# Performance work log

Measured on AMD Instinct MI355X. Metric: run time of the kernel, lower is better.

Reference implementation:

```python
import jax, jax.numpy as jnp
import numpy as np

N_HEADS = 8
N_LAYERS = 2
LN_EPS = 1e-5


def _mha(x, Win, bin_, Wout, bout):
    # torch nn.MultiheadAttention, eval mode (dropout off). x: [b, s, d]
    b, s, d = x.shape
    dh = d // N_HEADS
    qkv = x @ Win.T + bin_                      # [b, s, 3d]
    q, k, v = jnp.split(qkv, 3, axis=-1)
    q = q.reshape(b, s, N_HEADS, dh)
    k = k.reshape(b, s, N_HEADS, dh)
    v = v.reshape(b, s, N_HEADS, dh)
    scores = jnp.einsum('bqhd,bkhd->bhqk', q, k) / jnp.sqrt(jnp.asarray(dh, x.dtype))
    attn = jax.nn.softmax(scores, axis=-1)
    o = jnp.einsum('bhqk,bkhd->bqhd', attn, v).reshape(b, s, d)
    return o @ Wout.T + bout


def _layer_norm(x, g, b):
    mu = jnp.mean(x, axis=-1, keepdims=True)
    var = jnp.mean(jnp.square(x - mu), axis=-1, keepdims=True)
    return (x - mu) * jax.lax.rsqrt(var + LN_EPS) * g + b


def _vertex_conv(feat, inc, prev, Win, bin_, Wout, bout, Wproj, ln_g, ln_b, alpha):
    # feat: [b,m,d], inc: [b,m,e]
    attn = _mha(feat, Win, bin_, Wout, bout)              # [b,m,d]
    scores = jnp.einsum('bme,bmd->bed', inc, attn)        # incidence aggregation
    w = jax.nn.softmax(scores, axis=1)                    # softmax over edges
    # fused form of einsum('bme,bmd->bmed') then einsum('bmed,bed->bed')
    edge = scores * w                                     # [b,e,d]
    edge = edge @ Wproj.T                                 # no-bias projection
    edge = _layer_norm(edge, ln_g, ln_b)
    if prev is not None:
        edge = alpha * prev + (1.0 - alpha) * edge
        edge = edge + prev
    return edge


def _edge_conv(inc, edge_feat, prev, Win, bin_, Wout, bout, Wproj, ln_g, ln_b, alpha):
    # inc: [b,m,e], edge_feat: [b,e,d]
    _ = _mha(edge_feat, Win, bin_, Wout, bout)            # attn computed, output unused downstream
    wef = jnp.einsum('bed,bme->bmd', edge_feat, inc)      # edge->node aggregation
    node = wef @ Wproj.T
    node = _layer_norm(node, ln_g, ln_b)
    if prev is not None:
        node = alpha * prev + (1.0 - alpha) * node
        node = node + prev
    return node


def setup_inputs() -> dict:
    key = jax.random.key(0)
    ks = jax.random.split(key, 8)
    b, m, e, d = 8, 1024, 1536, 256
    s = 0.02
    return {
        'features': jax.random.normal(ks[0], (b, m, d), jnp.float32),
        'inc_mat': (jax.random.uniform(ks[1], (b, m, e), jnp.float32) < 0.05).astype(jnp.float32),
        'vc_Win': jax.random.normal(ks[2], (3 * d, d), jnp.float32) * s,
        'vc_bin': jnp.zeros((3 * d,), jnp.float32),
        'vc_Wout': jax.random.normal(ks[3], (d, d), jnp.float32) * s,
        'vc_bout': jnp.zeros((d,), jnp.float32),
        'vc_Wproj': jax.random.normal(ks[4], (d, d), jnp.float32) * s,
        'vc_ln_g': jnp.ones((d,), jnp.float32),
        'vc_ln_b': jnp.zeros((d,), jnp.float32),
        'vc_alpha': jnp.asarray(0.5, jnp.float32),
        'ec_Win': jax.random.normal(ks[5], (3 * d, d), jnp.float32) * s,
        'ec_bin': jnp.zeros((3 * d,), jnp.float32),
        'ec_Wout': jax.random.normal(ks[6], (d, d), jnp.float32) * s,
        'ec_bout': jnp.zeros((d,), jnp.float32),
        'ec_Wproj': jax.random.normal(ks[7], (d, d), jnp.float32) * s,
        'ec_ln_g': jnp.ones((d,), jnp.float32),
        'ec_ln_b': jnp.zeros((d,), jnp.float32),
        'ec_alpha': jnp.asarray(0.5, jnp.float32),
    }


def reference(features, inc_mat,
              vc_Win, vc_bin, vc_Wout, vc_bout, vc_Wproj, vc_ln_g, vc_ln_b, vc_alpha,
              ec_Win, ec_bin, ec_Wout, ec_bout, ec_Wproj, ec_ln_g, ec_ln_b, ec_alpha):
    vc = (vc_Win, vc_bin, vc_Wout, vc_bout, vc_Wproj, vc_ln_g, vc_ln_b, vc_alpha)
    ec = (ec_Win, ec_bin, ec_Wout, ec_bout, ec_Wproj, ec_ln_g, ec_ln_b, ec_alpha)
    edge_feats = _vertex_conv(features, inc_mat, None, *vc)
    node_feats = _edge_conv(inc_mat, edge_feats, features, *ec)
    for _ in range(N_LAYERS):  # shared weights across layers, as in the torch module
        edge_feats = _vertex_conv(features, inc_mat, edge_feats, *vc)
        node_feats = _edge_conv(inc_mat, edge_feats, node_feats, *ec)
    return node_feats, edge_feats, inc_mat
```

## Files before the change

kernel.cpp:

```cpp
#include <hip/hip_runtime.h>
#include <stdint.h>


#define DEV static __device__ __forceinline__

typedef __attribute__((ext_vector_type(8))) short bf16x8;
typedef __attribute__((ext_vector_type(4))) float f32x4;

DEV uint16_t f2bf(float x){
  union{float f; uint32_t u;} v; v.f=x;
  uint32_t r = v.u + 0x7fffu + ((v.u>>16)&1u);
  return (uint16_t)(r>>16);
}
DEV float bf2f(uint16_t b){
  union{uint32_t u; float f;} v; v.u=((uint32_t)b)<<16; return v.f;
}

#if __has_builtin(__builtin_amdgcn_global_load_lds)
#define HAVE_GLL 1
#else
#define HAVE_GLL 0
#endif

DEV void load_lds16(const uint16_t* g, void* l){
#if HAVE_GLL
  __builtin_amdgcn_global_load_lds((const __attribute__((address_space(1))) uint32_t*)g,
                                   (__attribute__((address_space(3))) uint32_t*)l, 16, 0, 0);
#else
  *(bf16x8*)l = *(const bf16x8*)g;
#endif
}

__global__ __launch_bounds__(256)
void cast_all(const float* __restrict__ feats, const float* __restrict__ win,
              const float* __restrict__ wout, const float* __restrict__ wpv,
              const float* __restrict__ wpe,
              uint16_t* __restrict__ xb, uint16_t* __restrict__ ow,
              uint16_t* __restrict__ oo, uint16_t* __restrict__ ov,
              uint16_t* __restrict__ oe){
  int i = blockIdx.x*256 + threadIdx.x;
  const float* src; uint16_t* dst; int j;
  if (i < 524288){ src=feats; dst=xb; j=i; }
  else {
    i -= 524288;
    if (i < 49152){ src=win; dst=ow; j=i; }
    else if (i < 65536){ src=wout; dst=oo; j=i-49152; }
    else if (i < 81920){ src=wpv; dst=ov; j=i-65536; }
    else { src=wpe; dst=oe; j=i-81920; }
  }
  float4 v = ((const float4*)src)[j];
  union { uint16_t u[4]; uint64_t q; } p;
  p.u[0]=f2bf(v.x); p.u[1]=f2bf(v.y); p.u[2]=f2bf(v.z); p.u[3]=f2bf(v.w);
  ((uint64_t*)dst)[j] = p.q;
}

__global__ __launch_bounds__(256)
void prep_inc(const float* __restrict__ inc, float* __restrict__ out_inc,
              uint16_t* __restrict__ incb, uint16_t* __restrict__ incT){
  __shared__ float T[32][33];
  int b = blockIdx.z;
  int c0 = blockIdx.x*32;
  int r0 = blockIdx.y*32;
  int tx = threadIdx.x, ty = threadIdx.y;
  size_t base = (size_t)b*1024*1536;
#pragma unroll
  for (int j=0;j<4;++j){
    int r = r0 + ty + j*8;
    size_t idx = base + (size_t)r*1536 + c0 + tx;
    float v = inc[idx];
    T[ty+j*8][tx] = v;
    out_inc[idx] = v;
    incb[idx] = f2bf(v);
  }
  __syncthreads();
  size_t baseT = (size_t)b*1536*1024;
#pragma unroll
  for (int j=0;j<4;++j){
    int c = c0 + ty + j*8;
    incT[baseT + (size_t)c*1024 + r0 + tx] = f2bf(T[tx][ty+j*8]);
  }
}

template<int WM, int BK, int EPI>
__global__ __launch_bounds__(256, 3)
void gemm_nt(const uint16_t* __restrict__ A, const uint16_t* __restrict__ B,
             float* __restrict__ Cf, uint16_t* __restrict__ Cb,
             const float* __restrict__ bias,
             int M, int N, int K, long sA, long sB, long sC,
             float* __restrict__ extra){
  constexpr int AROWS = WM*32;
  constexpr int UPR = BK/8;
  constexpr int RPP = 256/UPR;
  __shared__ short As[AROWS*BK];
  __shared__ short Bs[128*BK];
  const int tid = threadIdx.x;
  const int lane = tid & 63;
  const int w = tid >> 6;
  const int wm = w & 1, wn = w >> 1;
  const int r = lane & 15, q = lane >> 4;
  const long zb = blockIdx.z;
  const uint16_t* Ab = A + zb*sA + (size_t)(blockIdx.x*AROWS)*K;
  const uint16_t* Bb = B + zb*sB + (size_t)(blockIdx.y*128)*K;
  f32x4 acc[WM][4];
#pragma unroll
  for (int i=0;i<WM;++i)
#pragma unroll
    for (int j=0;j<4;++j) acc[i][j] = (f32x4){0.f,0.f,0.f,0.f};

  const int srow = tid / UPR;
  const int sblk = tid % UPR;

  for (int kb = 0; kb < K; kb += BK){
#pragma unroll
    for (int i=0;i<AROWS/RPP;++i){
      int row = srow + RPP*i;
      int lblk = sblk ^ (row & (UPR-1));
      load_lds16(Ab + (size_t)row*K + kb + lblk*8, (char*)As + i*4096 + tid*16);
    }
#pragma unroll
    for (int i=0;i<128/RPP;++i){
      int row = srow + RPP*i;
      int lblk = sblk ^ (row & (UPR-1));
      load_lds16(Bb + (size_t)row*K + kb + lblk*8, (char*)Bs + i*4096 + tid*16);
    }
    __syncthreads();
#pragma unroll
    for (int kc=0;kc<BK/32;++kc){
      bf16x8 af[WM], bf[4];
#pragma unroll
      for (int mt=0;mt<WM;++mt){
        int m = wm*(WM*16) + mt*16 + r;
        af[mt] = *(const bf16x8*)&As[m*BK + ((kc*4 + q) ^ (m&(UPR-1)))*8];
      }
#pragma unroll
      for (int nt=0;nt<4;++nt){
        int n = wn*64 + nt*16 + r;
        bf[nt] = *(const bf16x8*)&Bs[n*BK + ((kc*4 + q) ^ (n&(UPR-1)))*8];
      }
#pragma unroll
      for (int mt=0;mt<WM;++mt)
#pragma unroll
        for (int nt=0;nt<4;++nt)
          acc[mt][nt] = __builtin_amdgcn_mfma_f32_16x16x32_bf16(af[mt], bf[nt], acc[mt][nt], 0,0,0);
    }
    __syncthreads();
  }

  const int gm0 = blockIdx.x*AROWS + wm*(WM*16);
  const int gn0 = blockIdx.y*128 + wn*64;

  if constexpr (EPI == 1){
#pragma unroll
    for (int mt=0;mt<WM;++mt){
      int gmb = gm0 + mt*16 + q*4;
      size_t bb_ = (size_t)(gmb>>10)*(256*1024);
      int mm = gmb & 1023;
#pragma unroll
      for (int nt=0;nt<4;++nt){
        int gn = gn0 + nt*16 + r;
        float bv = bias ? bias[gn] : 0.f;
        union{uint16_t u[4]; uint64_t q64;} pk;
#pragma unroll
        for (int reg=0;reg<4;++reg) pk.u[reg] = f2bf(acc[mt][nt][reg] + bv);
        *(uint64_t*)(Cb + bb_ + (size_t)gn*1024 + mm) = pk.q64;
      }
    }
  } else {
#pragma unroll
    for (int mt=0;mt<WM;++mt){
#pragma unroll
      for (int nt=0;nt<4;++nt){
        int gn = gn0 + nt*16 + r;
        float bv = bias ? bias[gn] : 0.f;
#pragma unroll
        for (int reg=0;reg<4;++reg){
          int gm = gm0 + mt*16 + q*4 + reg;
          float v = acc[mt][nt][reg] + bv;
          size_t off = (size_t)(zb*sC) + (size_t)gm*N + gn;
          if (Cf) Cf[off] = v;
          if (Cb) Cb[off] = f2bf(v);
        }
      }
    }
    if constexpr (EPI == 2){
      __shared__ float colsum[2][128];
#pragma unroll
      for (int nt=0;nt<4;++nt){
        float s = 0.f;
#pragma unroll
        for (int mt=0;mt<WM;++mt)
#pragma unroll
          for (int reg=0;reg<4;++reg) s += __expf(acc[mt][nt][reg]);
        s += __shfl_xor(s, 16);
        s += __shfl_xor(s, 32);
        if (q == 0) colsum[wm][wn*64 + nt*16 + r] = s;
      }
      __syncthreads();
      if (tid < 128){
        float v = colsum[0][tid] + colsum[1][tid];
        extra[((size_t)zb*gridDim.x + blockIdx.x)*256 + blockIdx.y*128 + tid] = v;
      }
    }
  }
}

__global__ __launch_bounds__(256)
void reduce_L(const float* __restrict__ part, float* __restrict__ plinv){
  int b = blockIdx.x, d = threadIdx.x;
  float L = 0.f;
#pragma unroll
  for (int i=0;i<24;++i) L += part[((size_t)b*24 + i)*256 + d];
  plinv[b*256+d] = 1.0f / L;
}

template<int MODE>
__global__ __launch_bounds__(512, 4)
void gemm_ln(const uint16_t* __restrict__ A, const uint16_t* __restrict__ B,
             const float* __restrict__ g, const float* __restrict__ bb,
             const float* __restrict__ alpha, const float* __restrict__ feats,
             float* __restrict__ out, uint16_t* __restrict__ baset, int K){
  __shared__ short As[64*64];
  __shared__ short Bs[256*64];
  __shared__ float lnS[4][64], lnQ[4][64];
  const int tid = threadIdx.x;
  const int lane = tid & 63;
  const int w = tid >> 6;
  const int wm = w & 1;
  const int wn2 = w >> 1;
  const int r = lane & 15, q = lane >> 4;
  const uint16_t* Ab = A + (size_t)(blockIdx.x*64)*K;
  f32x4 acc[2][4];
#pragma unroll
  for (int i=0;i<2;++i)
#pragma unroll
    for (int j=0;j<4;++j) acc[i][j] = (f32x4){0.f,0.f,0.f,0.f};

  const int srow = tid >> 3;
  const int sblk = tid & 7;

  for (int kb = 0; kb < K; kb += 64){
    {
      int row = srow;
      int lblk = sblk ^ (row & 7);
      load_lds16(Ab + (size_t)row*K + kb + lblk*8, (char*)As + tid*16);
    }
#pragma unroll
    for (int i=0;i<4;++i){
      int row = srow + 64*i;
      int lblk = sblk ^ (row & 7);
      load_lds16(B + (size_t)row*K + kb + lblk*8, (char*)Bs + i*8192 + tid*16);
    }
    __syncthreads();
#pragma unroll
    for (int kc=0;kc<2;++kc){
      bf16x8 af[2], bf[4];
#pragma unroll
      for (int mt=0;mt<2;++mt){
        int m = wm*32 + mt*16 + r;
        af[mt] = *(const bf16x8*)&As[m*64 + ((kc*4 + q) ^ (m&7))*8];
      }
#pragma unroll
      for (int nt=0;nt<4;++nt){
        int n = wn2*64 + nt*16 + r;
        bf[nt] = *(const bf16x8*)&Bs[n*64 + ((kc*4 + q) ^ (n&7))*8];
      }
#pragma unroll
      for (int mt=0;mt<2;++mt)
#pragma unroll
        for (int nt=0;nt<4;++nt)
          acc[mt][nt] = __builtin_amdgcn_mfma_f32_16x16x32_bf16(af[mt], bf[nt], acc[mt][nt], 0,0,0);
    }
    __syncthreads();
  }

  float rs[2][4], rq[2][4];
#pragma unroll
  for (int mt=0;mt<2;++mt)
#pragma unroll
    for (int reg=0;reg<4;++reg){
      float s=0.f, s2=0.f;
#pragma unroll
      for (int nt=0;nt<4;++nt){
        float v = acc[mt][nt][reg];
        s += v; s2 += v*v;
      }
#pragma unroll
      for (int off=1; off<16; off<<=1){ s += __shfl_xor(s,off); s2 += __shfl_xor(s2,off); }
      rs[mt][reg]=s; rq[mt][reg]=s2;
    }
  if (r == 0){
#pragma unroll
    for (int mt=0;mt<2;++mt)
#pragma unroll
      for (int reg=0;reg<4;++reg){
        int row = wm*32 + mt*16 + q*4 + reg;
        lnS[wn2][row] = rs[mt][reg];
        lnQ[wn2][row] = rq[mt][reg];
      }
  }
  __syncthreads();

  const float a = alpha[0];
  float c0, c1;
  if constexpr (MODE == 0){ c0 = 3.0f + a; c1 = 0.f; }
  else {
    float ap1 = 1.f + a;
    c0 = (1.f - a)*(ap1*ap1 + ap1 + 1.f);
    c1 = ap1*ap1*ap1;
  }

  float mu_[2][4], rstd_[2][4];
#pragma unroll
  for (int mt=0;mt<2;++mt)
#pragma unroll
    for (int reg=0;reg<4;++reg){
      int row = wm*32 + mt*16 + q*4 + reg;
      float S = lnS[0][row]+lnS[1][row]+lnS[2][row]+lnS[3][row];
      float Q = lnQ[0][row]+lnQ[1][row]+lnQ[2][row]+lnQ[3][row];
      float mu = S * (1.f/256.f);
      float var = fmaxf(Q*(1.f/256.f) - mu*mu, 0.f);
      mu_[mt][reg] = mu;
      rstd_[mt][reg] = rsqrtf(var + 1e-5f);
    }

  int bb2 = blockIdx.x / 24;
  int e0  = (blockIdx.x % 24) * 64 + wm*32;

#pragma unroll
  for (int mt=0;mt<2;++mt){
#pragma unroll
    for (int nt=0;nt<4;++nt){
      int gn = wn2*64 + nt*16 + r;
      float gv = g[gn], bv = bb[gn];
      union{uint16_t u[4]; uint64_t q64;} pk;
#pragma unroll
      for (int reg=0;reg<4;++reg){
        int row = wm*32 + mt*16 + q*4 + reg;
        size_t gm = (size_t)blockIdx.x*64 + row;
        float nv = (acc[mt][nt][reg]-mu_[mt][reg])*rstd_[mt][reg]*gv + bv;
        float o;
        if constexpr (MODE == 0){ o = nv * c0; pk.u[reg] = f2bf(o); }
        else o = c1*feats[gm*256+gn] + c0*nv;
        out[gm*256 + gn] = o;
      }
      if constexpr (MODE == 0){
        int ee = e0 + mt*16 + q*4;
        *(uint64_t*)(baset + ((size_t)bb2*256 + gn)*1536 + ee) = pk.q64;
      }
    }
  }
}

DEV void stage_K(short* Kl, const uint16_t* __restrict__ qkv, size_t rowbase,
                 int c, int h, int kr){
  const uint16_t* kp = qkv + ((rowbase + c*256 + kr)*768 + 256 + h*32);
  int sz = (kr&3) ^ ((kr>>2)&1);
#pragma unroll
  for (int lb=0; lb<4; ++lb){
    bf16x8 v = *(const bf16x8*)(kp + lb*8);
    *(bf16x8*)&Kl[kr*32 + ((lb ^ sz))*8] = v;
  }
}

DEV void stage_V(short* VT, const uint16_t* __restrict__ qkv, size_t rowbase,
                 int c, int h, int t){
  int kvp = (t>>1)*2;
  int dhh = (t&1)*16;
  const uint16_t* v0 = qkv + ((rowbase + c*256 + kvp)*768 + 512 + h*32 + dhh);
  const uint16_t* v1 = v0 + 768;
  bf16x8 a0 = *(const bf16x8*)(v0);
  bf16x8 a1 = *(const bf16x8*)(v0+8);
  bf16x8 b0 = *(const bf16x8*)(v1);
  bf16x8 b1 = *(const bf16x8*)(v1+8);
  int blkbase = kvp>>3, off = kvp&7;
#pragma unroll
  for (int i=0;i<8;++i){
    int dh = dhh + i;
    uint32_t pack = (uint32_t)(uint16_t)a0[i] | ((uint32_t)(uint16_t)b0[i]<<16);
    *(uint32_t*)&VT[dh*256 + ((blkbase ^ (dh&7))*8) + off] = pack;
  }
#pragma unroll
  for (int i=0;i<8;++i){
    int dh = dhh + 8 + i;
    uint32_t pack = (uint32_t)(uint16_t)a1[i] | ((uint32_t)(uint16_t)b1[i]<<16);
    *(uint32_t*)&VT[dh*256 + ((blkbase ^ (dh&7))*8) + off] = pack;
  }
}

__global__ __launch_bounds__(512)
void attn_fwd(const uint16_t* __restrict__ qkv, uint16_t* __restrict__ O){
  __shared__ short Kl[256*32];
  __shared__ short VT[32*256];
  __shared__ short Pl[8][16*36];
  const int tid = threadIdx.x, lane = tid&63, w = tid>>6;
  const int r = lane&15, q = lane>>4;
  const int bh = blockIdx.y, b = bh>>3, h = bh&7;
  const int q0 = blockIdx.x*128 + w*16;
  const size_t rowbase = (size_t)b*1024;

  bf16x8 aq;
  {
    const float qscale = 0.17677669529663687f;
    const uint16_t* p = qkv + ((rowbase + q0 + r)*768 + h*32 + q*8);
    bf16x8 t = *(const bf16x8*)p;
#pragma unroll
    for (int j=0;j<8;++j)
      t[j] = (short)f2bf(bf2f((uint16_t)t[j]) * qscale);
    aq = t;
  }

  f32x4 o[2];
  o[0]=(f32x4){0.f,0.f,0.f,0.f}; o[1]=(f32x4){0.f,0.f,0.f,0.f};
  float l = 0.f;

  for (int c=0;c<4;++c){
    __syncthreads();
    if (tid < 256) stage_K(Kl, qkv, rowbase, c, h, tid);
    else           stage_V(VT, qkv, rowbase, c, h, tid-256);
    __syncthreads();
    for (int s32=0; s32<8; ++s32){
#pragma unroll
      for (int t2=0;t2<2;++t2){
        int rn = s32*32 + t2*16 + r;
        int sz = (rn&3) ^ ((rn>>2)&1);
        bf16x8 bk = *(const bf16x8*)&Kl[rn*32 + ((q ^ sz))*8];
        f32x4 z = (f32x4){0.f,0.f,0.f,0.f};
        f32x4 st = __builtin_amdgcn_mfma_f32_16x16x32_bf16(bk, aq, z, 0,0,0);
        union{uint16_t u[4]; uint64_t q64;} pk;
#pragma unroll
        for (int reg=0;reg<4;++reg){
          float p = __expf(st[reg]);
          l += p;
          pk.u[reg] = f2bf(p);
        }
        *(uint64_t*)&Pl[w][r*36 + t2*16 + q*4] = pk.q64;
      }
      bf16x8 bv[2];
#pragma unroll
      for (int db=0;db<2;++db){
        int dh = db*16 + r;
        bv[db] = *(const bf16x8*)&VT[dh*256 + (((s32*4 + q) ^ (dh&7)))*8];
      }
      bf16x8 ap = *(const bf16x8*)&Pl[w][r*36 + q*8];
#pragma unroll
      for (int db=0;db<2;++db)
        o[db] = __builtin_amdgcn_mfma_f32_16x16x32_bf16(ap, bv[db], o[db], 0,0,0);
    }
  }

  l += __shfl_xor(l, 16);
  l += __shfl_xor(l, 32);
#pragma unroll
  for (int db=0;db<2;++db)
#pragma unroll
    for (int reg=0;reg<4;++reg){
      float li = __shfl(l, q*4 + reg);
      int qr = q0 + q*4 + reg;
      O[(rowbase + qr)*256 + h*32 + db*16 + r] = f2bf(o[db][reg] / li);
    }
}

__global__ __launch_bounds__(256)
void edge_sm_apply(const float* __restrict__ scores, const float* __restrict__ plinv,
                   uint16_t* __restrict__ edgeb){
  int b = blockIdx.y;
  int i4 = blockIdx.x*256 + threadIdx.x;
  int e = i4>>6, d4 = (i4&63)*4;
  size_t off = ((size_t)b*1536 + e)*256 + d4;
  float4 v = *(const float4*)(scores + off);
  float4 Li = *(const float4*)(plinv + b*256 + d4);
  union{uint16_t u[4];uint64_t q;} p;
  p.u[0] = f2bf(v.x * __expf(v.x) * Li.x);
  p.u[1] = f2bf(v.y * __expf(v.y) * Li.y);
  p.u[2] = f2bf(v.z * __expf(v.z) * Li.z);
  p.u[3] = f2bf(v.w * __expf(v.w) * Li.w);
  *(uint64_t*)(edgeb + off) = p.q;
}

extern "C" void kernel_launch(void* const* d_in, const int* in_sizes, int n_in,
                              void* d_out, int out_size, void* d_ws, size_t ws_size,
                              hipStream_t stream){
  const float* features = (const float*)d_in[0];
  const float* inc      = (const float*)d_in[1];
  const float* vc_Win   = (const float*)d_in[2];
  const float* vc_bin   = (const float*)d_in[3];
  const float* vc_Wout  = (const float*)d_in[4];
  const float* vc_bout  = (const float*)d_in[5];
  const float* vc_Wproj = (const float*)d_in[6];
  const float* vc_ln_g  = (const float*)d_in[7];
  const float* vc_ln_b  = (const float*)d_in[8];
  const float* vc_alpha = (const float*)d_in[9];
  const float* ec_Wproj = (const float*)d_in[14];
  const float* ec_ln_g  = (const float*)d_in[15];
  const float* ec_ln_b  = (const float*)d_in[16];
  const float* ec_alpha = (const float*)d_in[17];

  float* out = (float*)d_out;
  float* out_node = out;
  float* out_edge = out + 2097152;
  float* out_inc  = out + 5242880;

  char* ws = (char*)d_ws;
  uint16_t* XB    = (uint16_t*)(ws + 0);
  float*    PART  = (float*)   (ws + 0);
  float*    PLINV = (float*)   (ws + 196608);
  uint16_t* WINB  = (uint16_t*)(ws + 4194304);
  uint16_t* WOUTB = (uint16_t*)(ws + 4587520);
  uint16_t* WPVB  = (uint16_t*)(ws + 4718592);
  uint16_t* WPEB  = (uint16_t*)(ws + 4849664);
  uint16_t* INCB  = (uint16_t*)(ws + 4988928);
  uint16_t* INCT  = (uint16_t*)(ws + 30154752);
  uint16_t* QKVB  = (uint16_t*)(ws + 55320576);
  float*    SCORES= (float*)   (ws + 55320576);
  uint16_t* OB    = (uint16_t*)(ws + 67903488);
  uint16_t* ATTNT = (uint16_t*)(ws + 72097792);
  uint16_t* EDGEB = (uint16_t*)(ws + 76292096);
  uint16_t* BASET = (uint16_t*)(ws + 82583552);
  uint16_t* W0B   = (uint16_t*)(ws + 88875008);

  cast_all<<<2432,256,0,stream>>>(features, vc_Win, vc_Wout, vc_Wproj, ec_Wproj,
                                  XB, WINB, WOUTB, WPVB, WPEB);
  prep_inc<<<dim3(48,32,8), dim3(32,8), 0, stream>>>(inc, out_inc, INCB, INCT);

  gemm_nt<4,64,0><<<dim3(64,6,1),256,0,stream>>>(XB, WINB, nullptr, QKVB, vc_bin,
                                                 8192,768,256, 0,0,0, nullptr);
  attn_fwd<<<dim3(8,64),512,0,stream>>>(QKVB, OB);
  gemm_nt<2,128,1><<<dim3(128,2,1),256,0,stream>>>(OB, WOUTB, nullptr, ATTNT, vc_bout,
                                                   8192,256,256, 0,0,0, nullptr);

  gemm_nt<2,128,2><<<dim3(24,2,8),256,0,stream>>>(INCT, ATTNT, SCORES, nullptr, nullptr,
                                                  1536,256,1024,
                                                  1536L*1024, 256L*1024, 1536L*256, PART);
  reduce_L<<<8,256,0,stream>>>(PART, PLINV);
  edge_sm_apply<<<dim3(384,8),256,0,stream>>>(SCORES, PLINV, EDGEB);

  gemm_ln<0><<<192,512,0,stream>>>(EDGEB, WPVB, vc_ln_g, vc_ln_b, vc_alpha,
                                   nullptr, out_edge, BASET, 256);

  gemm_nt<2,128,0><<<dim3(16,2,8),256,0,stream>>>(INCB, BASET, nullptr, W0B, nullptr,
                                                  1024,256,1536,
                                                  1024L*1536, 256L*1536, 1024L*256, nullptr);
  gemm_ln<1><<<128,512,0,stream>>>(W0B, WPEB, ec_ln_g, ec_ln_b, ec_alpha,
                                   features, out_node, nullptr, 256);
}
```

Before: 274.2 us.

## Fuse edge softmax and partial-sum reduction into LN GEMM; merge prep kernels

```diff
diff --git a/kernel.cpp b/kernel.cpp
--- a/kernel.cpp
+++ b/kernel.cpp
@@ -32,52 +32,56 @@
 }
 
 __global__ __launch_bounds__(256)
-void cast_all(const float* __restrict__ feats, const float* __restrict__ win,
-              const float* __restrict__ wout, const float* __restrict__ wpv,
-              const float* __restrict__ wpe,
-              uint16_t* __restrict__ xb, uint16_t* __restrict__ ow,
-              uint16_t* __restrict__ oo, uint16_t* __restrict__ ov,
-              uint16_t* __restrict__ oe){
-  int i = blockIdx.x*256 + threadIdx.x;
-  const float* src; uint16_t* dst; int j;
-  if (i < 524288){ src=feats; dst=xb; j=i; }
-  else {
-    i -= 524288;
-    if (i < 49152){ src=win; dst=ow; j=i; }
-    else if (i < 65536){ src=wout; dst=oo; j=i-49152; }
-    else if (i < 81920){ src=wpv; dst=ov; j=i-65536; }
-    else { src=wpe; dst=oe; j=i-81920; }
-  }
-  float4 v = ((const float4*)src)[j];
-  union { uint16_t u[4]; uint64_t q; } p;
-  p.u[0]=f2bf(v.x); p.u[1]=f2bf(v.y); p.u[2]=f2bf(v.z); p.u[3]=f2bf(v.w);
-  ((uint64_t*)dst)[j] = p.q;
-}
-
-__global__ __launch_bounds__(256)
-void prep_inc(const float* __restrict__ inc, float* __restrict__ out_inc,
-              uint16_t* __restrict__ incb, uint16_t* __restrict__ incT){
+void prep(const float* __restrict__ inc, float* __restrict__ out_inc,
+          uint16_t* __restrict__ incb, uint16_t* __restrict__ incT,
+          const float* __restrict__ feats, const float* __restrict__ win,
+          const float* __restrict__ wout, const float* __restrict__ wpv,
+          const float* __restrict__ wpe,
+          uint16_t* __restrict__ xb, uint16_t* __restrict__ ow,
+          uint16_t* __restrict__ oo, uint16_t* __restrict__ ov,
+          uint16_t* __restrict__ oe){
   __shared__ float T[32][33];
-  int b = blockIdx.z;
-  int c0 = blockIdx.x*32;
-  int r0 = blockIdx.y*32;
-  int tx = threadIdx.x, ty = threadIdx.y;
-  size_t base = (size_t)b*1024*1536;
-#pragma unroll
-  for (int j=0;j<4;++j){
-    int r = r0 + ty + j*8;
-    size_t idx = base + (size_t)r*1536 + c0 + tx;
-    float v = inc[idx];
-    T[ty+j*8][tx] = v;
-    out_inc[idx] = v;
-    incb[idx] = f2bf(v);
-  }
-  __syncthreads();
-  size_t baseT = (size_t)b*1536*1024;
-#pragma unroll
-  for (int j=0;j<4;++j){
-    int c = c0 + ty + j*8;
-    incT[baseT + (size_t)c*1024 + r0 + tx] = f2bf(T[tx][ty+j*8]);
+  int bx = blockIdx.x;
+  int tid = threadIdx.x;
+  if (bx < 12288){
+    int x = bx % 48;
+    int t = bx / 48;
+    int y = t % 32;
+    int b = t / 32;
+    int c0 = x*32, r0 = y*32;
+    int tx = tid & 31, ty = tid >> 5;
+    size_t base = (size_t)b*1024*1536;
+#pragma unroll
+    for (int j=0;j<4;++j){
+      int r = r0 + ty + j*8;
+      size_t idx = base + (size_t)r*1536 + c0 + tx;
+      float v = inc[idx];
+      T[ty+j*8][tx] = v;
+      out_inc[idx] = v;
+      incb[idx] = f2bf(v);
+    }
+    __syncthreads();
+    size_t baseT = (size_t)b*1536*1024;
+#pragma unroll
+    for (int j=0;j<4;++j){
+      int c = c0 + ty + j*8;
+      incT[baseT + (size_t)c*1024 + r0 + tx] = f2bf(T[tx][ty+j*8]);
+    }
+  } else {
+    int i = (bx - 12288)*256 + tid;
+    const float* src; uint16_t* dst; int j;
+    if (i < 524288){ src=feats; dst=xb; j=i; }
+    else {
+      i -= 524288;
+      if (i < 49152){ src=win; dst=ow; j=i; }
+      else if (i < 65536){ src=wout; dst=oo; j=i-49152; }
+      else if (i < 81920){ src=wpv; dst=ov; j=i-65536; }
+      else { src=wpe; dst=oe; j=i-81920; }
+    }
+    float4 v = ((const float4*)src)[j];
+    union { uint16_t u[4]; uint64_t q; } p;
+    p.u[0]=f2bf(v.x); p.u[1]=f2bf(v.y); p.u[2]=f2bf(v.z); p.u[3]=f2bf(v.w);
+    ((uint64_t*)dst)[j] = p.q;
   }
 }
 
@@ -204,21 +208,154 @@
   }
 }
 
-__global__ __launch_bounds__(256)
-void reduce_L(const float* __restrict__ part, float* __restrict__ plinv){
-  int b = blockIdx.x, d = threadIdx.x;
-  float L = 0.f;
-#pragma unroll
-  for (int i=0;i<24;++i) L += part[((size_t)b*24 + i)*256 + d];
-  plinv[b*256+d] = 1.0f / L;
-}
-
-template<int MODE>
 __global__ __launch_bounds__(512, 4)
-void gemm_ln(const uint16_t* __restrict__ A, const uint16_t* __restrict__ B,
-             const float* __restrict__ g, const float* __restrict__ bb,
-             const float* __restrict__ alpha, const float* __restrict__ feats,
-             float* __restrict__ out, uint16_t* __restrict__ baset, int K){
+void gemm_ln_edge(const uint16_t* __restrict__ SB, const uint16_t* __restrict__ B,
+                  const float* __restrict__ part, const float* __restrict__ g,
+                  const float* __restrict__ bb, const float* __restrict__ alpha,
+                  float* __restrict__ out, uint16_t* __restrict__ baset){
+  __shared__ short As[64*64];
+  __shared__ short Bs[256*64];
+  __shared__ float lnS[4][64], lnQ[4][64];
+  __shared__ float PLinv[256];
+  __shared__ float Phalf[2][256];
+  const int tid = threadIdx.x;
+  const int lane = tid & 63;
+  const int w = tid >> 6;
+  const int wm = w & 1;
+  const int wn2 = w >> 1;
+  const int r = lane & 15, q = lane >> 4;
+  const int batch = blockIdx.x / 24;
+
+  {
+    int d = tid & 255, h = tid >> 8;
+    float s = 0.f;
+#pragma unroll
+    for (int i=0;i<12;++i) s += part[((size_t)batch*24 + h*12 + i)*256 + d];
+    Phalf[h][d] = s;
+  }
+  __syncthreads();
+  if (tid < 256) PLinv[tid] = 1.0f / (Phalf[0][tid] + Phalf[1][tid]);
+  __syncthreads();
+
+  f32x4 acc[2][4];
+#pragma unroll
+  for (int i=0;i<2;++i)
+#pragma unroll
+    for (int j=0;j<4;++j) acc[i][j] = (f32x4){0.f,0.f,0.f,0.f};
+
+  const int srow = tid >> 3;
+  const int sblk = tid & 7;
+
+  for (int kb = 0; kb < 256; kb += 64){
+    {
+      bf16x8 v = *(const bf16x8*)(SB + (size_t)(blockIdx.x*64 + srow)*256 + kb + sblk*8);
+      const float* Lp = &PLinv[kb + sblk*8];
+      bf16x8 pv;
+#pragma unroll
+      for (int j=0;j<8;++j){
+        float x = bf2f((uint16_t)v[j]);
+        pv[j] = (short)f2bf(x * __expf(x) * Lp[j]);
+      }
+      *(bf16x8*)&As[srow*64 + (sblk ^ (srow&7))*8] = pv;
+    }
+#pragma unroll
+    for (int i=0;i<4;++i){
+      int row = srow + 64*i;
+      int lblk = sblk ^ (row & 7);
+      load_lds16(B + (size_t)row*256 + kb + lblk*8, (char*)Bs + i*8192 + tid*16);
+    }
+    __syncthreads();
+#pragma unroll
+    for (int kc=0;kc<2;++kc){
+      bf16x8 af[2], bf[4];
+#pragma unroll
+      for (int mt=0;mt<2;++mt){
+        int m = wm*32 + mt*16 + r;
+        af[mt] = *(const bf16x8*)&As[m*64 + ((kc*4 + q) ^ (m&7))*8];
+      }
+#pragma unroll
+      for (int nt=0;nt<4;++nt){
+        int n = wn2*64 + nt*16 + r;
+        bf[nt] = *(const bf16x8*)&Bs[n*64 + ((kc*4 + q) ^ (n&7))*8];
+      }
+#pragma unroll
+      for (int mt=0;mt<2;++mt)
+#pragma unroll
+        for (int nt=0;nt<4;++nt)
+          acc[mt][nt] = __builtin_amdgcn_mfma_f32_16x16x32_bf16(af[mt], bf[nt], acc[mt][nt], 0,0,0);
+    }
+    __syncthreads();
+  }
+
+  float rs[2][4], rq[2][4];
+#pragma unroll
+  for (int mt=0;mt<2;++mt)
+#pragma unroll
+    for (int reg=0;reg<4;++reg){
+      float s=0.f, s2=0.f;
+#pragma unroll
+      for (int nt=0;nt<4;++nt){
+        float v = acc[mt][nt][reg];
+        s += v; s2 += v*v;
+      }
+#pragma unroll
+      for (int off=1; off<16; off<<=1){ s += __shfl_xor(s,off); s2 += __shfl_xor(s2,off); }
+      rs[mt][reg]=s; rq[mt][reg]=s2;
+    }
+  if (r == 0){
+#pragma unroll
+    for (int mt=0;mt<2;++mt)
+#pragma unroll
+      for (int reg=0;reg<4;++reg){
+        int row = wm*32 + mt*16 + q*4 + reg;
+        lnS[wn2][row] = rs[mt][reg];
+        lnQ[wn2][row] = rq[mt][reg];
+      }
+  }
+  __syncthreads();
+
+  const float c0 = 3.0f + alpha[0];
+  float mu_[2][4], rstd_[2][4];
+#pragma unroll
+  for (int mt=0;mt<2;++mt)
+#pragma unroll
+    for (int reg=0;reg<4;++reg){
+      int row = wm*32 + mt*16 + q*4 + reg;
+      float S = lnS[0][row]+lnS[1][row]+lnS[2][row]+lnS[3][row];
+      float Q = lnQ[0][row]+lnQ[1][row]+lnQ[2][row]+lnQ[3][row];
+      float mu = S * (1.f/256.f);
+      float var = fmaxf(Q*(1.f/256.f) - mu*mu, 0.f);
+      mu_[mt][reg] = mu;
+      rstd_[mt][reg] = rsqrtf(var + 1e-5f);
+    }
+
+  int e0 = (blockIdx.x % 24) * 64 + wm*32;
+#pragma unroll
+  for (int mt=0;mt<2;++mt){
+#pragma unroll
+    for (int nt=0;nt<4;++nt){
+      int gn = wn2*64 + nt*16 + r;
+      float gv = g[gn], bv = bb[gn];
+      union{uint16_t u[4]; uint64_t q64;} pk;
+#pragma unroll
+      for (int reg=0;reg<4;++reg){
+        int row = wm*32 + mt*16 + q*4 + reg;
+        size_t gm = (size_t)blockIdx.x*64 + row;
+        float o = ((acc[mt][nt][reg]-mu_[mt][reg])*rstd_[mt][reg]*gv + bv) * c0;
+        pk.u[reg] = f2bf(o);
+        out[gm*256 + gn] = o;
+      }
+      int ee = e0 + mt*16 + q*4;
+      *(uint64_t*)(baset + ((size_t)batch*256 + gn)*1536 + ee) = pk.q64;
+    }
+  }
+}
+
+__global__ __launch_bounds__(512, 4)
+void gemm_ln_node(const uint16_t* __restrict__ A, const uint16_t* __restrict__ B,
+                  const float* __restrict__ g, const float* __restrict__ bb,
+                  const float* __restrict__ alpha, const float* __restrict__ feats,
+                  float* __restrict__ out){
   __shared__ short As[64*64];
   __shared__ short Bs[256*64];
   __shared__ float lnS[4][64], lnQ[4][64];
@@ -228,7 +365,7 @@
   const int wm = w & 1;
   const int wn2 = w >> 1;
   const int r = lane & 15, q = lane >> 4;
-  const uint16_t* Ab = A + (size_t)(blockIdx.x*64)*K;
+  const uint16_t* Ab = A + (size_t)(blockIdx.x*64)*256;
   f32x4 acc[2][4];
 #pragma unroll
   for (int i=0;i<2;++i)
@@ -238,17 +375,16 @@
   const int srow = tid >> 3;
   const int sblk = tid & 7;
 
-  for (int kb = 0; kb < K; kb += 64){
+  for (int kb = 0; kb < 256; kb += 64){
     {
-      int row = srow;
-      int lblk = sblk ^ (row & 7);
-      load_lds16(Ab + (size_t)row*K + kb + lblk*8, (char*)As + tid*16);
+      int lblk = sblk ^ (srow & 7);
+      load_lds16(Ab + (size_t)srow*256 + kb + lblk*8, (char*)As + tid*16);
     }
 #pragma unroll
     for (int i=0;i<4;++i){
       int row = srow + 64*i;
       int lblk = sblk ^ (row & 7);
-      load_lds16(B + (size_t)row*K + kb + lblk*8, (char*)Bs + i*8192 + tid*16);
+      load_lds16(B + (size_t)row*256 + kb + lblk*8, (char*)Bs + i*8192 + tid*16);
     }
     __syncthreads();
 #pragma unroll
@@ -301,17 +437,12 @@
   __syncthreads();
 
   const float a = alpha[0];
-  float c0, c1;
-  if constexpr (MODE == 0){ c0 = 3.0f + a; c1 = 0.f; }
-  else {
-    float ap1 = 1.f + a;
-    c0 = (1.f - a)*(ap1*ap1 + ap1 + 1.f);
-    c1 = ap1*ap1*ap1;
-  }
-
-  float mu_[2][4], rstd_[2][4];
-#pragma unroll
-  for (int mt=0;mt<2;++mt)
+  const float ap1 = 1.f + a;
+  const float cn = (1.f - a)*(ap1*ap1 + ap1 + 1.f);
+  const float cf = ap1*ap1*ap1;
+
+#pragma unroll
+  for (int mt=0;mt<2;++mt){
 #pragma unroll
     for (int reg=0;reg<4;++reg){
       int row = wm*32 + mt*16 + q*4 + reg;
@@ -319,33 +450,13 @@
       float Q = lnQ[0][row]+lnQ[1][row]+lnQ[2][row]+lnQ[3][row];
       float mu = S * (1.f/256.f);
       float var = fmaxf(Q*(1.f/256.f) - mu*mu, 0.f);
-      mu_[mt][reg] = mu;
-      rstd_[mt][reg] = rsqrtf(var + 1e-5f);
-    }
-
-  int bb2 = blockIdx.x / 24;
-  int e0  = (blockIdx.x % 24) * 64 + wm*32;
-
-#pragma unroll
-  for (int mt=0;mt<2;++mt){
-#pragma unroll
-    for (int nt=0;nt<4;++nt){
-      int gn = wn2*64 + nt*16 + r;
-      float gv = g[gn], bv = bb[gn];
-      union{uint16_t u[4]; uint64_t q64;} pk;
-#pragma unroll
-      for (int reg=0;reg<4;++reg){
-        int row = wm*32 + mt*16 + q*4 + reg;
-        size_t gm = (size_t)blockIdx.x*64 + row;
-        float nv = (acc[mt][nt][reg]-mu_[mt][reg])*rstd_[mt][reg]*gv + bv;
-        float o;
-        if constexpr (MODE == 0){ o = nv * c0; pk.u[reg] = f2bf(o); }
-        else o = c1*feats[gm*256+gn] + c0*nv;
-        out[gm*256 + gn] = o;
-      }
-      if constexpr (MODE == 0){
-        int ee = e0 + mt*16 + q*4;
-        *(uint64_t*)(baset + ((size_t)bb2*256 + gn)*1536 + ee) = pk.q64;
+      float rstd = rsqrtf(var + 1e-5f);
+      size_t gm = (size_t)blockIdx.x*64 + row;
+#pragma unroll
+      for (int nt=0;nt<4;++nt){
+        int gn = wn2*64 + nt*16 + r;
+        float nv = (acc[mt][nt][reg]-mu)*rstd*g[gn] + bb[gn];
+        out[gm*256 + gn] = cf*feats[gm*256+gn] + cn*nv;
       }
     }
   }
@@ -458,23 +569,6 @@
       int qr = q0 + q*4 + reg;
       O[(rowbase + qr)*256 + h*32 + db*16 + r] = f2bf(o[db][reg] / li);
     }
-}
-
-__global__ __launch_bounds__(256)
-void edge_sm_apply(const float* __restrict__ scores, const float* __restrict__ plinv,
-                   uint16_t* __restrict__ edgeb){
-  int b = blockIdx.y;
-  int i4 = blockIdx.x*256 + threadIdx.x;
-  int e = i4>>6, d4 = (i4&63)*4;
-  size_t off = ((size_t)b*1536 + e)*256 + d4;
-  float4 v = *(const float4*)(scores + off);
-  float4 Li = *(const float4*)(plinv + b*256 + d4);
-  union{uint16_t u[4];uint64_t q;} p;
-  p.u[0] = f2bf(v.x * __expf(v.x) * Li.x);
-  p.u[1] = f2bf(v.y * __expf(v.y) * Li.y);
-  p.u[2] = f2bf(v.z * __expf(v.z) * Li.z);
-  p.u[3] = f2bf(v.w * __expf(v.w) * Li.w);
-  *(uint64_t*)(edgeb + off) = p.q;
 }
 
 extern "C" void kernel_launch(void* const* d_in, const int* in_sizes, int n_in,
@@ -501,26 +595,24 @@
   float* out_inc  = out + 5242880;
 
   char* ws = (char*)d_ws;
-  uint16_t* XB    = (uint16_t*)(ws + 0);
-  float*    PART  = (float*)   (ws + 0);
-  float*    PLINV = (float*)   (ws + 196608);
-  uint16_t* WINB  = (uint16_t*)(ws + 4194304);
-  uint16_t* WOUTB = (uint16_t*)(ws + 4587520);
-  uint16_t* WPVB  = (uint16_t*)(ws + 4718592);
-  uint16_t* WPEB  = (uint16_t*)(ws + 4849664);
-  uint16_t* INCB  = (uint16_t*)(ws + 4988928);
-  uint16_t* INCT  = (uint16_t*)(ws + 30154752);
-  uint16_t* QKVB  = (uint16_t*)(ws + 55320576);
-  float*    SCORES= (float*)   (ws + 55320576);
-  uint16_t* OB    = (uint16_t*)(ws + 67903488);
-  uint16_t* ATTNT = (uint16_t*)(ws + 72097792);
-  uint16_t* EDGEB = (uint16_t*)(ws + 76292096);
-  uint16_t* BASET = (uint16_t*)(ws + 82583552);
-  uint16_t* W0B   = (uint16_t*)(ws + 88875008);
-
-  cast_all<<<2432,256,0,stream>>>(features, vc_Win, vc_Wout, vc_Wproj, ec_Wproj,
-                                  XB, WINB, WOUTB, WPVB, WPEB);
-  prep_inc<<<dim3(48,32,8), dim3(32,8), 0, stream>>>(inc, out_inc, INCB, INCT);
+  uint16_t* XB     = (uint16_t*)(ws + 0);
+  float*    PART   = (float*)   (ws + 0);
+  uint16_t* WINB   = (uint16_t*)(ws + 4194304);
+  uint16_t* WOUTB  = (uint16_t*)(ws + 4587520);
+  uint16_t* WPVB   = (uint16_t*)(ws + 4718592);
+  uint16_t* WPEB   = (uint16_t*)(ws + 4849664);
+  uint16_t* INCB   = (uint16_t*)(ws + 4988928);
+  uint16_t* INCT   = (uint16_t*)(ws + 30154752);
+  uint16_t* QKVB   = (uint16_t*)(ws + 55320576);
+  uint16_t* SCORESB= (uint16_t*)(ws + 55320576);
+  uint16_t* OB     = (uint16_t*)(ws + 67903488);
+  uint16_t* ATTNT  = (uint16_t*)(ws + 72097792);
+  uint16_t* BASET  = (uint16_t*)(ws + 82583552);
+  uint16_t* W0B    = (uint16_t*)(ws + 88875008);
+
+  prep<<<14720,256,0,stream>>>(inc, out_inc, INCB, INCT,
+                               features, vc_Win, vc_Wout, vc_Wproj, ec_Wproj,
+                               XB, WINB, WOUTB, WPVB, WPEB);
 
   gemm_nt<4,64,0><<<dim3(64,6,1),256,0,stream>>>(XB, WINB, nullptr, QKVB, vc_bin,
                                                  8192,768,256, 0,0,0, nullptr);
@@ -528,18 +620,16 @@
   gemm_nt<2,128,1><<<dim3(128,2,1),256,0,stream>>>(OB, WOUTB, nullptr, ATTNT, vc_bout,
                                                    8192,256,256, 0,0,0, nullptr);
 
-  gemm_nt<2,128,2><<<dim3(24,2,8),256,0,stream>>>(INCT, ATTNT, SCORES, nullptr, nullptr,
+  gemm_nt<2,128,2><<<dim3(24,2,8),256,0,stream>>>(INCT, ATTNT, nullptr, SCORESB, nullptr,
                                                   1536,256,1024,
                                                   1536L*1024, 256L*1024, 1536L*256, PART);
-  reduce_L<<<8,256,0,stream>>>(PART, PLINV);
-  edge_sm_apply<<<dim3(384,8),256,0,stream>>>(SCORES, PLINV, EDGEB);
-
-  gemm_ln<0><<<192,512,0,stream>>>(EDGEB, WPVB, vc_ln_g, vc_ln_b, vc_alpha,
-                                   nullptr, out_edge, BASET, 256);
+
+  gemm_ln_edge<<<192,512,0,stream>>>(SCORESB, WPVB, PART, vc_ln_g, vc_ln_b,
+                                     vc_alpha, out_edge, BASET);
 
   gemm_nt<2,128,0><<<dim3(16,2,8),256,0,stream>>>(INCB, BASET, nullptr, W0B, nullptr,
                                                   1024,256,1536,
                                                   1024L*1536, 256L*1536, 1024L*256, nullptr);
-  gemm_ln<1><<<128,512,0,stream>>>(W0B, WPEB, ec_ln_g, ec_ln_b, ec_alpha,
-                                   features, out_node, nullptr, 256);
-}
+  gemm_ln_node<<<128,512,0,stream>>>(W0B, WPEB, ec_ln_g, ec_ln_b, ec_alpha,
+                                     features, out_node);
+}
```

Measured after the change: 264.6 us, median of 2. -3.5%, faster.
